# Performance work log

Measured on AMD Instinct MI355X. Metric: run time of the kernel, lower is better.

The kernel has to match this reference:

```python
import jax, jax.numpy as jnp
import numpy as np

EPS = 1e-5  # BatchNorm eps; eval-mode BN with running_mean=0, running_var=1 -> affine


def pe3d(C, x, y, z):
    """PositionalEncoding3D -> (C, x, y, z), faithfully reproducing the torch
    broadcasting (emb_x of shape (x,1,c) assigned into (x,y,z,c) slices)."""
    c = int(np.ceil(C / 3))
    inv_freq = jnp.asarray(1.0 / (10000.0 ** (np.arange(0, c, 2, dtype=np.float32) / c)))
    def emb(n):
        s = jnp.arange(n, dtype=jnp.float32)[:, None] * inv_freq[None, :]
        return jnp.concatenate([jnp.sin(s), jnp.cos(s)], axis=-1)  # (n, c)
    ex = emb(x)[:, None, :]   # (x,1,c) -> broadcasts as (1,x,1,c), same as torch
    ey = emb(y)[:, None, :]   # (y,1,c)
    ez = emb(z)               # (z,c)
    out = jnp.zeros((x, y, z, 3 * c), dtype=jnp.float32)
    out = out.at[..., :c].set(ex)
    out = out.at[..., c:2 * c].set(ey)
    out = out.at[..., 2 * c:3 * c].set(ez)
    return jnp.transpose(out[..., :C], (3, 0, 1, 2))  # (C,x,y,z)


def conv1x1(x, w, b):  # x:(B,Ci,D,H,W) w:(Co,Ci)
    return jnp.einsum('bcdhw,oc->bodhw', x, w) + b[None, :, None, None, None]


def bn_relu(x, g, b):  # eval BN (mean 0, var 1) + ReLU
    s = g / jnp.sqrt(1.0 + EPS)
    return jax.nn.relu(x * s[None, :, None, None, None] + b[None, :, None, None, None])


def setup_inputs() -> dict:
    key = jax.random.key(0)
    ks = jax.random.split(key, 16)
    B, Cy, Cs, D, H, W = 2, 96, 48, 16, 16, 16
    w = lambda k, shp: jax.random.normal(k, shp, dtype=jnp.float32) * 0.05
    return {
        'Y': jax.random.normal(ks[0], (B, Cy, D, H, W), dtype=jnp.float32),
        'S': jax.random.normal(ks[1], (B, Cs, D, H, W), dtype=jnp.float32),
        'w_s': w(ks[2], (Cs, Cs)), 'b_s': jnp.zeros((Cs,), jnp.float32),
        'g_s': jnp.ones((Cs,), jnp.float32), 'be_s': jnp.zeros((Cs,), jnp.float32),
        'w_y': w(ks[3], (Cs, Cy)), 'b_y': jnp.zeros((Cs,), jnp.float32),
        'g_y': jnp.ones((Cs,), jnp.float32), 'be_y': jnp.zeros((Cs,), jnp.float32),
        'Wq': w(ks[4], (Cs, Cs)), 'Wk': w(ks[5], (Cs, Cs)), 'Wv': w(ks[6], (Cs, Cs)),
        'w_o': w(ks[7], (Cs, Cs)), 'b_o': jnp.zeros((Cs,), jnp.float32),
        'g_o': jnp.ones((Cs,), jnp.float32), 'be_o': jnp.zeros((Cs,), jnp.float32),
        'w3': w(ks[8], (Cy, Cy, 3, 3, 3)), 'b3': jnp.zeros((Cy,), jnp.float32),
        'w_y2': w(ks[9], (Cs, Cy)), 'b_y2': jnp.zeros((Cs,), jnp.float32),
        'g_y2': jnp.ones((Cs,), jnp.float32), 'be_y2': jnp.zeros((Cs,), jnp.float32),
    }


def reference(Y, S, w_s, b_s, g_s, be_s, w_y, b_y, g_y, be_y, Wq, Wk, Wv,
              w_o, b_o, g_o, be_o, w3, b3, w_y2, b_y2, g_y2, be_y2):
    B, Cs, D, H, W = S.shape
    Cy = Y.shape[1]
    N = D * H * W
    # positional encodings (added, not learned)
    S = S + pe3d(Cs, D, H, W)[None]
    Y = Y + pe3d(Cy, D, H, W)[None]
    # projections: conv1x1 + BN + ReLU
    S1 = bn_relu(conv1x1(S, w_s, b_s), g_s, be_s).reshape(B, Cs, N).transpose(0, 2, 1)  # (B,N,Cs)
    Y1 = bn_relu(conv1x1(Y, w_y, b_y), g_y, be_y).reshape(B, Cs, N).transpose(0, 2, 1)  # (B,N,Cs)
    # Yconv2: 3x3x3 conv -> 1x1 conv -> BN -> ReLU
    Y3 = jax.lax.conv_general_dilated(Y, w3, (1, 1, 1), 'SAME',
                                      dimension_numbers=('NCDHW', 'OIDHW', 'NCDHW'))
    Y3 = Y3 + b3[None, :, None, None, None]
    Y2 = bn_relu(conv1x1(Y3, w_y2, b_y2), g_y2, be_y2)  # (B,Cs,D,H,W)
    # MultiHeadDense = plain right-matmul by (d,d) weight
    Q = jnp.einsum('bnd,de->bne', Y1, Wq)
    K = jnp.einsum('bnd,de->bne', Y1, Wk)
    V = jnp.einsum('bnd,de->bne', S1, Wv)
    # attention with NON-STANDARD softmax over axis=1 (queries, not keys)
    A = jax.nn.softmax(jnp.einsum('bqd,bkd->bqk', Q, K) * (float(Cs) ** -0.5), axis=1)
    x = jnp.einsum('bqk,bkd->bqd', A, V)                       # (B,N,Cs)
    x = x.transpose(0, 2, 1).reshape(B, Cs, D, H, W)
    Z = bn_relu(conv1x1(x, w_o, b_o), g_o, be_o) * S
    return jnp.concatenate([Z, Y2], axis=1)  # (B, 2*Cs, D, H, W)
```

## Files before the change

### kernel.cpp

```cpp
#include <hip/hip_runtime.h>
#include <hip/hip_bf16.h>

#define NPOS 4096
#define BB 2
#define KS2 32
#define QS2 32

typedef short v4s __attribute__((ext_vector_type(4)));
typedef short v8s __attribute__((ext_vector_type(8)));
typedef float v4f __attribute__((ext_vector_type(4)));
typedef unsigned short ushort_t;

static __device__ __forceinline__ unsigned short f2bf(float f) {
    unsigned int u = __float_as_uint(f);
    return (unsigned short)((u + 0x7fffu + ((u >> 16) & 1u)) >> 16);
}
static __device__ __forceinline__ float bf2f(ushort_t s) {
    return __uint_as_float(((unsigned int)s) << 16);
}

__device__ __forceinline__ float pe_val(int C, int c, int ch, int h, int w) {
    int blk = ch / c;
    int j = ch - blk * c;
    int half = c >> 1;
    int jj = (j < half) ? j : j - half;
    float freq = __expf(-(2.0f * jj / (float)c) * 9.210340371976184f);
    int pos = (blk < 2) ? h : w;
    float s = (float)pos * freq;
    return (j < half) ? __sinf(s) : __cosf(s);
}

__global__ void prep1_kernel(const float* __restrict__ S, const float* __restrict__ Y,
                             const float* __restrict__ w3, float* __restrict__ S_pe,
                             float* __restrict__ Y_pe, ushort_t* __restrict__ wr) {
    int bid = blockIdx.x;
    if (bid < 1536) {
        int idx = bid * 256 + threadIdx.x;
        int n = idx & 4095; int ch = (idx >> 12) % 48;
        S_pe[idx] = S[idx] + pe_val(48, 16, ch, (n >> 4) & 15, n & 15);
    } else if (bid < 4608) {
        int idx = (bid - 1536) * 256 + threadIdx.x;
        int n = idx & 4095; int ch = (idx >> 12) % 96;
        Y_pe[idx] = Y[idx] + pe_val(96, 32, ch, (n >> 4) & 15, n & 15);
    } else {
        int idx = (bid - 4608) * 256 + threadIdx.x;
        if (idx < 27 * 96 * 96) {
            int ci = idx % 96;
            int t2 = idx / 96;
            int co = t2 % 96;
            int tap = t2 / 96;
            wr[idx] = f2bf(w3[(size_t)(co * 96 + ci) * 27 + tap]);
        }
    }
}

template<int CI>
__device__ __forceinline__ void proj_body(int r, const float* __restrict__ in,
                                          const float* __restrict__ w, const float* __restrict__ bias,
                                          const float* __restrict__ g, const float* __restrict__ be,
                                          float* __restrict__ out) {
    int pc = r >> 3, cc = r & 7;
    int o0 = cc * 6;
    __shared__ float wl[6 * CI];
    __shared__ float sb[6], bb[6];
    int t = threadIdx.x;
    for (int i = t; i < 6 * CI; i += 256) {
        int o = i / CI, ci = i - o * CI;
        wl[i] = w[(size_t)(o0 + o) * CI + ci];
    }
    if (t < 6) {
        float s = g[o0 + t] * rsqrtf(1.0f + 1e-5f);
        sb[t] = s; bb[t] = bias[o0 + t] * s + be[o0 + t];
    }
    __syncthreads();
    int gn = pc * 256 + t;
    int b = gn >> 12;
    const float* ip = in + (size_t)b * CI * NPOS + (gn & 4095);
    float acc[6];
#pragma unroll
    for (int o = 0; o < 6; o++) acc[o] = 0.f;
#pragma unroll
    for (int ci = 0; ci < CI; ci++) {
        float v = ip[(size_t)ci * NPOS];
#pragma unroll
        for (int o = 0; o < 6; o++) acc[o] += v * wl[o * CI + ci];
    }
    float* op = out + (size_t)gn * 48 + o0;
#pragma unroll
    for (int o = 0; o < 6; o++) {
        float z = acc[o] * sb[o] + bb[o];
        op[o] = z > 0.f ? z : 0.f;
    }
}

__global__ void prep2_kernel(const float* __restrict__ Y_pe, const float* __restrict__ S_pe,
                             const float* __restrict__ w_s, const float* __restrict__ b_s,
                             const float* __restrict__ g_s, const float* __restrict__ be_s,
                             const float* __restrict__ w_y, const float* __restrict__ b_y,
                             const float* __restrict__ g_y, const float* __restrict__ be_y,
                             ushort_t* __restrict__ Ypad, float* __restrict__ S1,
                             float* __restrict__ Y1) {
    int bid = blockIdx.x;
    if (bid < 1094) {
        int idx = bid * 256 + threadIdx.x;
        if (idx >= BB * 5832 * 24) return;
        int ci4 = idx % 24;
        int cell = idx / 24;
        int wp = cell % 18; int c2 = cell / 18;
        int hp = c2 % 18; int c3 = c2 / 18;
        int zp = c3 % 18; int b = c3 / 18;
        ushort_t pk[4] = {0, 0, 0, 0};
        if (zp >= 1 && zp <= 16 && hp >= 1 && hp <= 16 && wp >= 1 && wp <= 16) {
            int n = (zp - 1) * 256 + (hp - 1) * 16 + (wp - 1);
#pragma unroll
            for (int j = 0; j < 4; j++)
                pk[j] = f2bf(Y_pe[((size_t)(b * 96 + ci4 * 4 + j) << 12) + n]);
        }
        *(v4s*)&Ypad[(size_t)idx * 4] = *(v4s*)pk;
    } else {
        int r = bid - 1094;
        if (r < 256) proj_body<48>(r, S_pe, w_s, b_s, g_s, be_s, S1);
        else proj_body<96>(r - 256, Y_pe, w_y, b_y, g_y, be_y, Y1);
    }
}

__global__ void qkv_kernel(const float* __restrict__ Y1, const float* __restrict__ S1,
                           const float* __restrict__ Wq, const float* __restrict__ Wk,
                           const float* __restrict__ Wv, ushort_t* __restrict__ Qb,
                           ushort_t* __restrict__ Kb, ushort_t* __restrict__ Vt) {
    int grp = blockIdx.x >> 8;
    int r = blockIdx.x & 255;
    int pc = r >> 3, cc = r & 7;
    int o0 = cc * 6;
    const float* in = (grp == 2) ? S1 : Y1;
    const float* w = (grp == 0) ? Wq : (grp == 1) ? Wk : Wv;
    __shared__ float wl[48 * 6];
    int t = threadIdx.x;
    for (int i = t; i < 48 * 6; i += 256) {
        int d = i / 6, o = i - d * 6;
        wl[i] = w[(size_t)d * 48 + o0 + o];
    }
    __syncthreads();
    int gn = pc * 256 + t;
    const float* ip = in + (size_t)gn * 48;
    float acc[6];
#pragma unroll
    for (int o = 0; o < 6; o++) acc[o] = 0.f;
#pragma unroll
    for (int d = 0; d < 48; d++) {
        float v = ip[d];
#pragma unroll
        for (int o = 0; o < 6; o++) acc[o] += v * wl[d * 6 + o];
    }
    if (grp < 2) {
        ushort_t* base = (grp == 0 ? Qb : Kb) + (size_t)gn * 64;
#pragma unroll
        for (int o = 0; o < 6; o++) base[o0 + o] = f2bf(acc[o]);
        if (cc == 0) {
            v8s z = {0, 0, 0, 0, 0, 0, 0, 0};
            *(v8s*)(base + 48) = z;
            *(v8s*)(base + 56) = z;
        }
    } else {
        int b = gn >> 12; int n = gn & 4095;
#pragma unroll
        for (int o = 0; o < 6; o++)
            Vt[((size_t)(b * 48 + o0 + o) << 12) + n] = f2bf(acc[o]);
    }
}

__global__ void attn_stats_mfma_kernel(const ushort_t* __restrict__ Qb,
                                       const ushort_t* __restrict__ Kb,
                                       float* __restrict__ ps) {
    int bid = blockIdx.x;
    int qs = bid & 31; int kb = (bid >> 5) & 15; int b = bid >> 9;
    int t = threadIdx.x; int wv = t >> 6; int lane = t & 63;
    int lr = lane & 15, g = lane >> 4;
    const float scale = 0.14433756729740643f;
    int key0 = kb * 256 + wv * 64;
    v8s ka[4][2];
#pragma unroll
    for (int kt = 0; kt < 4; kt++) {
        const ushort_t* krow = Kb + ((size_t)(b * NPOS + key0 + kt * 16 + lr)) * 64;
        ka[kt][0] = *(const v8s*)(krow + 8 * g);
        ka[kt][1] = *(const v8s*)(krow + 32 + 8 * g);
    }
    float s[4][4];
#pragma unroll
    for (int kt = 0; kt < 4; kt++)
#pragma unroll
        for (int r = 0; r < 4; r++) s[kt][r] = 0.f;
    for (int qt = 0; qt < 8; qt++) {
        int q = qs * 128 + qt * 16 + lr;
        const ushort_t* qrow = Qb + ((size_t)(b * NPOS + q)) * 64;
        v8s qf0 = *(const v8s*)(qrow + 8 * g);
        v8s qf1 = *(const v8s*)(qrow + 32 + 8 * g);
#pragma unroll
        for (int kt = 0; kt < 4; kt++) {
            v4f acc = {0.f, 0.f, 0.f, 0.f};
            acc = __builtin_amdgcn_mfma_f32_16x16x32_bf16(ka[kt][0], qf0, acc, 0, 0, 0);
            acc = __builtin_amdgcn_mfma_f32_16x16x32_bf16(ka[kt][1], qf1, acc, 0, 0, 0);
#pragma unroll
            for (int r = 0; r < 4; r++) s[kt][r] += __expf(acc[r] * scale);
        }
    }
#pragma unroll
    for (int off = 1; off < 16; off <<= 1)
#pragma unroll
        for (int kt = 0; kt < 4; kt++)
#pragma unroll
            for (int r = 0; r < 4; r++) s[kt][r] += __shfl_xor(s[kt][r], off);
    if (lr == 0) {
#pragma unroll
        for (int kt = 0; kt < 4; kt++) {
            int idx = (b * QS2 + qs) * NPOS + key0 + kt * 16 + 4 * g;
            v4f ss = {s[kt][0], s[kt][1], s[kt][2], s[kt][3]};
            *(v4f*)&ps[idx] = ss;
        }
    }
}

__global__ void norm_vscale_kernel(const float* __restrict__ ps, ushort_t* __restrict__ Vt) {
    int idx = blockIdx.x * 256 + threadIdx.x;
    if (idx >= BB * 4 * NPOS) return;
    int k = idx & 4095;
    int rest = idx >> 12;
    int dg = rest & 3; int b = rest >> 2;
    float s = 0.f;
#pragma unroll
    for (int qs = 0; qs < QS2; qs++) s += ps[(size_t)(b * QS2 + qs) * NPOS + k];
    float ci = 1.0f / s;
#pragma unroll
    for (int d = dg * 12; d < dg * 12 + 12; d++) {
        size_t a = ((size_t)(b * 48 + d) << 12) + k;
        Vt[a] = f2bf(bf2f(Vt[a]) * ci);
    }
}

__global__ void attn_pv_mfma_kernel(const ushort_t* __restrict__ Qb,
                                    const ushort_t* __restrict__ Kb,
                                    const ushort_t* __restrict__ Vt,
                                    ushort_t* __restrict__ xpart) {
    int bid = blockIdx.x;
    int ks = bid & 31; int qb = (bid >> 5) & 15; int b = bid >> 9;
    int t = threadIdx.x; int wv = t >> 6; int lane = t & 63;
    int lr = lane & 15, g = lane >> 4;
    const float scale = 0.14433756729740643f;
    int q0 = qb * 256 + wv * 64;
    v8s qf[4][2];
#pragma unroll
    for (int qt = 0; qt < 4; qt++) {
        const ushort_t* qrow = Qb + ((size_t)(b * NPOS + q0 + qt * 16 + lr)) * 64;
        qf[qt][0] = *(const v8s*)(qrow + 8 * g);
        qf[qt][1] = *(const v8s*)(qrow + 32 + 8 * g);
    }
    v4f xacc[4][3];
#pragma unroll
    for (int qt = 0; qt < 4; qt++)
#pragma unroll
        for (int nt = 0; nt < 3; nt++) xacc[qt][nt] = (v4f){0.f, 0.f, 0.f, 0.f};
    for (int kt = 0; kt < 2; kt++) {
        int kb0 = ks * 128 + kt * 64;
        v4s p[4][4];
#pragma unroll
        for (int tm = 0; tm < 4; tm++) {
            const ushort_t* krow = Kb + ((size_t)(b * NPOS + kb0 + 16 * tm + lr)) * 64;
            v8s ka0 = *(const v8s*)(krow + 8 * g);
            v8s ka1 = *(const v8s*)(krow + 32 + 8 * g);
#pragma unroll
            for (int qt = 0; qt < 4; qt++) {
                v4f acc = {0.f, 0.f, 0.f, 0.f};
                acc = __builtin_amdgcn_mfma_f32_16x16x32_bf16(ka0, qf[qt][0], acc, 0, 0, 0);
                acc = __builtin_amdgcn_mfma_f32_16x16x32_bf16(ka1, qf[qt][1], acc, 0, 0, 0);
                v4s pp;
#pragma unroll
                for (int r = 0; r < 4; r++)
                    pp[r] = (short)f2bf(__expf(acc[r] * scale));
                p[tm][qt] = pp;
            }
        }
#pragma unroll
        for (int nt = 0; nt < 3; nt++) {
            const ushort_t* vrow = Vt + ((size_t)(b * 48 + 16 * nt + lr) << 12) + kb0;
#pragma unroll
            for (int tm = 0; tm < 4; tm++) {
                v4s vf = *(const v4s*)(vrow + 16 * tm + 4 * g);
#pragma unroll
                for (int qt = 0; qt < 4; qt++)
                    xacc[qt][nt] = __builtin_amdgcn_mfma_f32_16x16x16bf16_1k(
                        p[tm][qt], vf, xacc[qt][nt], 0, 0, 0);
            }
        }
    }
#pragma unroll
    for (int qt = 0; qt < 4; qt++)
#pragma unroll
        for (int nt = 0; nt < 3; nt++)
#pragma unroll
            for (int r = 0; r < 4; r++)
                xpart[(((size_t)(b * KS2 + ks) << 12) + q0 + qt * 16 + 4 * g + r) * 48 + 16 * nt + lr] =
                    f2bf(xacc[qt][nt][r]);
}

__global__ void xreduce_kernel(const ushort_t* __restrict__ xpart, float* __restrict__ xsum) {
    int v = blockIdx.x * 256 + threadIdx.x;
    if (v >= BB * NPOS * 6) return;
    int b = v / (NPOS * 6);
    int rem8 = (v - b * NPOS * 6) * 8;
    float s[8];
#pragma unroll
    for (int j = 0; j < 8; j++) s[j] = 0.f;
    const ushort_t* base = xpart + (size_t)b * KS2 * NPOS * 48 + rem8;
#pragma unroll 4
    for (int ks = 0; ks < KS2; ks++) {
        v8s x = *(const v8s*)(base + (size_t)ks * NPOS * 48);
#pragma unroll
        for (int j = 0; j < 8; j++) s[j] += bf2f((ushort_t)x[j]);
    }
    float* op = xsum + (size_t)b * NPOS * 48 + rem8;
    v4f lo = {s[0], s[1], s[2], s[3]};
    v4f hi = {s[4], s[5], s[6], s[7]};
    *(v4f*)op = lo;
    *(v4f*)(op + 4) = hi;
}

__global__ __launch_bounds__(256, 2)
void conv3d_mfma_kernel(const ushort_t* __restrict__ Ypad,
                        const ushort_t* __restrict__ wr,
                        const float* __restrict__ b3,
                        float* __restrict__ Y3) {
    int bid = blockIdx.x;
    int b = bid / 384;
    int r = bid % 384;
    int cot = r % 6;
    int zhq = r / 6;
    int t = threadIdx.x; int wv = t >> 6; int lane = t & 63;
    int z = zhq >> 2;
    int h = (zhq & 3) * 4 + wv;
    int lr = lane & 15, g = lane >> 4;
    v4f acc[3];
#pragma unroll
    for (int kd = 0; kd < 3; kd++) acc[kd] = (v4f){0.f, 0.f, 0.f, 0.f};
    const ushort_t* wbase = wr + (size_t)(cot * 16 + lr) * 96 + 8 * g;
#pragma unroll
    for (int kd = 0; kd < 3; kd++) {
#pragma unroll
        for (int kh = 0; kh < 3; kh++) {
            const ushort_t* arow = Ypad + (((size_t)(b * 18 + z + kd) * 18 + h + kh) * 18 + lr) * 96 + 8 * g;
            int tap0 = (kd * 3 + kh) * 3;
            v8s af[3][3], bf[3][3];
#pragma unroll
            for (int kw = 0; kw < 3; kw++)
#pragma unroll
                for (int c = 0; c < 3; c++) {
                    af[kw][c] = *(const v8s*)(arow + kw * 96 + c * 32);
                    bf[kw][c] = *(const v8s*)(wbase + (size_t)(tap0 + kw) * 96 * 96 + c * 32);
                }
#pragma unroll
            for (int kw = 0; kw < 3; kw++)
#pragma unroll
                for (int c = 0; c < 3; c++)
                    acc[kd] = __builtin_amdgcn_mfma_f32_16x16x32_bf16(
                        af[kw][c], bf[kw][c], acc[kd], 0, 0, 0);
        }
    }
    float bv = b3[cot * 16 + lr];
    int pos = z * 256 + h * 16 + 4 * g;
#pragma unroll
    for (int r2 = 0; r2 < 4; r2++)
        Y3[(((size_t)b << 12) + pos + r2) * 96 + cot * 16 + lr] =
            acc[0][r2] + acc[1][r2] + acc[2][r2] + bv;
}

__device__ __forceinline__ void z_out_body(int r, const float* __restrict__ xsum,
                                           const float* __restrict__ w_o, const float* __restrict__ b_o,
                                           const float* __restrict__ g_o, const float* __restrict__ be_o,
                                           const float* __restrict__ S_pe, float* __restrict__ out) {
    int pc = r >> 3, cc = r & 7;
    int o0 = cc * 6;
    __shared__ float wl[6 * 48];
    __shared__ float sb[6], bb[6];
    int t = threadIdx.x;
    for (int i = t; i < 6 * 48; i += 256) {
        int o = i / 48, d = i - o * 48;
        wl[i] = w_o[(size_t)(o0 + o) * 48 + d];
    }
    if (t < 6) {
        float s = g_o[o0 + t] * rsqrtf(1.f + 1e-5f);
        sb[t] = s; bb[t] = b_o[o0 + t] * s + be_o[o0 + t];
    }
    __syncthreads();
    int gn = pc * 256 + t;
    int b = gn >> 12; int n = gn & 4095;
    const v4f* p = (const v4f*)(xsum + (size_t)gn * 48);
    float x[48];
#pragma unroll
    for (int d4 = 0; d4 < 12; d4++) {
        v4f v = p[d4];
#pragma unroll
        for (int j = 0; j < 4; j++) x[d4 * 4 + j] = v[j];
    }
#pragma unroll
    for (int o = 0; o < 6; o++) {
        float acc = 0.f;
#pragma unroll
        for (int d = 0; d < 48; d++) acc += wl[o * 48 + d] * x[d];
        float z = acc * sb[o] + bb[o];
        z = z > 0.f ? z : 0.f;
        out[((size_t)b * 96 + o0 + o) * NPOS + n] = z * S_pe[((size_t)b * 48 + o0 + o) * NPOS + n];
    }
}

__device__ __forceinline__ void y2_out_body(int r, const float* __restrict__ Y3,
                                            const float* __restrict__ w_y2, const float* __restrict__ b_y2,
                                            const float* __restrict__ g_y2, const float* __restrict__ be_y2,
                                            float* __restrict__ out) {
    int pc = r >> 3, cc = r & 7;
    int o0 = cc * 6;
    __shared__ float wl2[6 * 96];
    __shared__ float sb2[6], bb2[6];
    int t = threadIdx.x;
    for (int i = t; i < 6 * 96; i += 256) {
        int o = i / 96, ci = i - o * 96;
        wl2[i] = w_y2[(size_t)(o0 + o) * 96 + ci];
    }
    if (t < 6) {
        float s = g_y2[o0 + t] * rsqrtf(1.f + 1e-5f);
        sb2[t] = s; bb2[t] = b_y2[o0 + t] * s + be_y2[o0 + t];
    }
    __syncthreads();
    int gn = pc * 256 + t;
    int b = gn >> 12; int n = gn & 4095;
    const v4f* ip = (const v4f*)(Y3 + (size_t)gn * 96);
    float acc[6];
#pragma unroll
    for (int o = 0; o < 6; o++) acc[o] = 0.f;
#pragma unroll
    for (int c4 = 0; c4 < 24; c4++) {
        v4f v = ip[c4];
#pragma unroll
        for (int j = 0; j < 4; j++)
#pragma unroll
            for (int o = 0; o < 6; o++) acc[o] += v[j] * wl2[o * 96 + c4 * 4 + j];
    }
#pragma unroll
    for (int o = 0; o < 6; o++) {
        float z = acc[o] * sb2[o] + bb2[o];
        out[((size_t)b * 96 + 48 + o0 + o) * NPOS + n] = z > 0.f ? z : 0.f;
    }
}

__global__ void zy_out_kernel(const float* __restrict__ xsum, const float* __restrict__ w_o,
                              const float* __restrict__ b_o, const float* __restrict__ g_o,
                              const float* __restrict__ be_o, const float* __restrict__ S_pe,
                              const float* __restrict__ Y3, const float* __restrict__ w_y2,
                              const float* __restrict__ b_y2, const float* __restrict__ g_y2,
                              const float* __restrict__ be_y2, float* __restrict__ out) {
    int bid = blockIdx.x;
    if (bid < 256) z_out_body(bid, xsum, w_o, b_o, g_o, be_o, S_pe, out);
    else y2_out_body(bid - 256, Y3, w_y2, b_y2, g_y2, be_y2, out);
}

extern "C" void kernel_launch(void* const* d_in, const int* in_sizes, int n_in,
                              void* d_out, int out_size, void* d_ws, size_t ws_size,
                              hipStream_t stream) {
    const float* Y    = (const float*)d_in[0];
    const float* S    = (const float*)d_in[1];
    const float* w_s  = (const float*)d_in[2];
    const float* b_s  = (const float*)d_in[3];
    const float* g_s  = (const float*)d_in[4];
    const float* be_s = (const float*)d_in[5];
    const float* w_y  = (const float*)d_in[6];
    const float* b_y  = (const float*)d_in[7];
    const float* g_y  = (const float*)d_in[8];
    const float* be_y = (const float*)d_in[9];
    const float* Wq   = (const float*)d_in[10];
    const float* Wk   = (const float*)d_in[11];
    const float* Wv   = (const float*)d_in[12];
    const float* w_o  = (const float*)d_in[13];
    const float* b_o  = (const float*)d_in[14];
    const float* g_o  = (const float*)d_in[15];
    const float* be_o = (const float*)d_in[16];
    const float* w3   = (const float*)d_in[17];
    const float* b3   = (const float*)d_in[18];
    const float* w_y2 = (const float*)d_in[19];
    const float* b_y2 = (const float*)d_in[20];
    const float* g_y2 = (const float*)d_in[21];
    const float* be_y2= (const float*)d_in[22];
    float* out = (float*)d_out;

    float* ws = (float*)d_ws;
    float* S_pe   = ws;
    float* Y_pe   = ws + 393216;
    float* S1     = ws + 1179648;
    float* Y1     = ws + 1572864;
    ushort_t* Qb  = (ushort_t*)(ws + 1966080);
    ushort_t* Kb  = (ushort_t*)(ws + 2228224);
    ushort_t* Vt  = (ushort_t*)(ws + 2490368);
    float* ps     = ws + 2686976;
    ushort_t* xpart = (ushort_t*)(ws + 2949120);
    float* xsum   = ws + 9240576;
    float* Y3     = ws + 9633792;
    ushort_t* Ypad= (ushort_t*)(ws + 10420224);
    ushort_t* wr  = (ushort_t*)(ws + 10980096);

    prep1_kernel<<<5580, 256, 0, stream>>>(S, Y, w3, S_pe, Y_pe, wr);
    prep2_kernel<<<1606, 256, 0, stream>>>(Y_pe, S_pe, w_s, b_s, g_s, be_s,
                                           w_y, b_y, g_y, be_y, Ypad, S1, Y1);
    qkv_kernel<<<768, 256, 0, stream>>>(Y1, S1, Wq, Wk, Wv, Qb, Kb, Vt);
    attn_stats_mfma_kernel<<<BB * 16 * QS2, 256, 0, stream>>>(Qb, Kb, ps);
    norm_vscale_kernel<<<128, 256, 0, stream>>>(ps, Vt);
    attn_pv_mfma_kernel<<<BB * 16 * KS2, 256, 0, stream>>>(Qb, Kb, Vt, xpart);
    conv3d_mfma_kernel<<<768, 256, 0, stream>>>(Ypad, wr, b3, Y3);
    xreduce_kernel<<<192, 256, 0, stream>>>(xpart, xsum);
    zy_out_kernel<<<512, 256, 0, stream>>>(xsum, w_o, b_o, g_o, be_o, S_pe,
                                           Y3, w_y2, b_y2, g_y2, be_y2, out);
}
```

Measured before the change: 139.6 us.

## Merge attention PV and 3D conv into one launch; vectorize positional-encoding prep

The attention PV kernel and the 3x3x3 conv kernel become device functions dispatched by block index from a single launch. The two are independent, so their blocks can share the GPU and one launch boundary is removed. The prep kernel now handles four elements per thread with float4 loads and stores, and builds a small per-block table of positional-encoding values in shared memory instead of calling sin/cos for every element. In exchange, the merged kernel takes on the conv's launch bounds (256, 2) for the PV path too, which could change register allocation there.

```diff
diff --git a/kernel.cpp b/kernel.cpp
--- a/kernel.cpp
+++ b/kernel.cpp
@@ -34,16 +34,44 @@
                              const float* __restrict__ w3, float* __restrict__ S_pe,
                              float* __restrict__ Y_pe, ushort_t* __restrict__ wr) {
     int bid = blockIdx.x;
-    if (bid < 1536) {
-        int idx = bid * 256 + threadIdx.x;
-        int n = idx & 4095; int ch = (idx >> 12) % 48;
-        S_pe[idx] = S[idx] + pe_val(48, 16, ch, (n >> 4) & 15, n & 15);
-    } else if (bid < 4608) {
-        int idx = (bid - 1536) * 256 + threadIdx.x;
-        int n = idx & 4095; int ch = (idx >> 12) % 96;
-        Y_pe[idx] = Y[idx] + pe_val(96, 32, ch, (n >> 4) & 15, n & 15);
+    int t = threadIdx.x;
+    __shared__ float tb[16];
+    if (bid < 384) {
+        int idx4 = bid * 256 + t;
+        int ch = (idx4 >> 10) % 48;
+        if (t < 16) tb[t] = pe_val(48, 16, ch, t, t);
+        __syncthreads();
+        int n = (idx4 & 1023) * 4;
+        int h = (n >> 4) & 15, w0 = n & 15;
+        v4f x = *(const v4f*)&S[(size_t)idx4 * 4];
+        if (ch < 32) {
+            float p = tb[h];
+#pragma unroll
+            for (int j = 0; j < 4; j++) x[j] += p;
+        } else {
+#pragma unroll
+            for (int j = 0; j < 4; j++) x[j] += tb[w0 + j];
+        }
+        *(v4f*)&S_pe[(size_t)idx4 * 4] = x;
+    } else if (bid < 1152) {
+        int idx4 = (bid - 384) * 256 + t;
+        int ch = (idx4 >> 10) % 96;
+        if (t < 16) tb[t] = pe_val(96, 32, ch, t, t);
+        __syncthreads();
+        int n = (idx4 & 1023) * 4;
+        int h = (n >> 4) & 15, w0 = n & 15;
+        v4f x = *(const v4f*)&Y[(size_t)idx4 * 4];
+        if (ch < 64) {
+            float p = tb[h];
+#pragma unroll
+            for (int j = 0; j < 4; j++) x[j] += p;
+        } else {
+#pragma unroll
+            for (int j = 0; j < 4; j++) x[j] += tb[w0 + j];
+        }
+        *(v4f*)&Y_pe[(size_t)idx4 * 4] = x;
     } else {
-        int idx = (bid - 4608) * 256 + threadIdx.x;
+        int idx = (bid - 1152) * 256 + t;
         if (idx < 27 * 96 * 96) {
             int ci = idx % 96;
             int t2 = idx / 96;
@@ -237,11 +265,10 @@
     }
 }
 
-__global__ void attn_pv_mfma_kernel(const ushort_t* __restrict__ Qb,
-                                    const ushort_t* __restrict__ Kb,
-                                    const ushort_t* __restrict__ Vt,
-                                    ushort_t* __restrict__ xpart) {
-    int bid = blockIdx.x;
+__device__ __forceinline__ void pv_body(int bid, const ushort_t* __restrict__ Qb,
+                                        const ushort_t* __restrict__ Kb,
+                                        const ushort_t* __restrict__ Vt,
+                                        ushort_t* __restrict__ xpart) {
     int ks = bid & 31; int qb = (bid >> 5) & 15; int b = bid >> 9;
     int t = threadIdx.x; int wv = t >> 6; int lane = t & 63;
     int lr = lane & 15, g = lane >> 4;
@@ -302,34 +329,10 @@
                     f2bf(xacc[qt][nt][r]);
 }
 
-__global__ void xreduce_kernel(const ushort_t* __restrict__ xpart, float* __restrict__ xsum) {
-    int v = blockIdx.x * 256 + threadIdx.x;
-    if (v >= BB * NPOS * 6) return;
-    int b = v / (NPOS * 6);
-    int rem8 = (v - b * NPOS * 6) * 8;
-    float s[8];
-#pragma unroll
-    for (int j = 0; j < 8; j++) s[j] = 0.f;
-    const ushort_t* base = xpart + (size_t)b * KS2 * NPOS * 48 + rem8;
-#pragma unroll 4
-    for (int ks = 0; ks < KS2; ks++) {
-        v8s x = *(const v8s*)(base + (size_t)ks * NPOS * 48);
-#pragma unroll
-        for (int j = 0; j < 8; j++) s[j] += bf2f((ushort_t)x[j]);
-    }
-    float* op = xsum + (size_t)b * NPOS * 48 + rem8;
-    v4f lo = {s[0], s[1], s[2], s[3]};
-    v4f hi = {s[4], s[5], s[6], s[7]};
-    *(v4f*)op = lo;
-    *(v4f*)(op + 4) = hi;
-}
-
-__global__ __launch_bounds__(256, 2)
-void conv3d_mfma_kernel(const ushort_t* __restrict__ Ypad,
-                        const ushort_t* __restrict__ wr,
-                        const float* __restrict__ b3,
-                        float* __restrict__ Y3) {
-    int bid = blockIdx.x;
+__device__ __forceinline__ void conv_body(int bid, const ushort_t* __restrict__ Ypad,
+                                          const ushort_t* __restrict__ wr,
+                                          const float* __restrict__ b3,
+                                          float* __restrict__ Y3) {
     int b = bid / 384;
     int r = bid % 384;
     int cot = r % 6;
@@ -370,6 +373,38 @@
     for (int r2 = 0; r2 < 4; r2++)
         Y3[(((size_t)b << 12) + pos + r2) * 96 + cot * 16 + lr] =
             acc[0][r2] + acc[1][r2] + acc[2][r2] + bv;
+}
+
+__global__ __launch_bounds__(256, 2)
+void pvconv_kernel(const ushort_t* __restrict__ Qb, const ushort_t* __restrict__ Kb,
+                   const ushort_t* __restrict__ Vt, ushort_t* __restrict__ xpart,
+                   const ushort_t* __restrict__ Ypad, const ushort_t* __restrict__ wr,
+                   const float* __restrict__ b3, float* __restrict__ Y3) {
+    int bid = blockIdx.x;
+    if (bid < BB * 16 * KS2) pv_body(bid, Qb, Kb, Vt, xpart);
+    else conv_body(bid - BB * 16 * KS2, Ypad, wr, b3, Y3);
+}
+
+__global__ void xreduce_kernel(const ushort_t* __restrict__ xpart, float* __restrict__ xsum) {
+    int v = blockIdx.x * 256 + threadIdx.x;
+    if (v >= BB * NPOS * 6) return;
+    int b = v / (NPOS * 6);
+    int rem8 = (v - b * NPOS * 6) * 8;
+    float s[8];
+#pragma unroll
+    for (int j = 0; j < 8; j++) s[j] = 0.f;
+    const ushort_t* base = xpart + (size_t)b * KS2 * NPOS * 48 + rem8;
+#pragma unroll 4
+    for (int ks = 0; ks < KS2; ks++) {
+        v8s x = *(const v8s*)(base + (size_t)ks * NPOS * 48);
+#pragma unroll
+        for (int j = 0; j < 8; j++) s[j] += bf2f((ushort_t)x[j]);
+    }
+    float* op = xsum + (size_t)b * NPOS * 48 + rem8;
+    v4f lo = {s[0], s[1], s[2], s[3]};
+    v4f hi = {s[4], s[5], s[6], s[7]};
+    *(v4f*)op = lo;
+    *(v4f*)(op + 4) = hi;
 }
 
 __device__ __forceinline__ void z_out_body(int r, const float* __restrict__ xsum,
@@ -504,14 +539,14 @@
     ushort_t* Ypad= (ushort_t*)(ws + 10420224);
     ushort_t* wr  = (ushort_t*)(ws + 10980096);
 
-    prep1_kernel<<<5580, 256, 0, stream>>>(S, Y, w3, S_pe, Y_pe, wr);
+    prep1_kernel<<<2124, 256, 0, stream>>>(S, Y, w3, S_pe, Y_pe, wr);
     prep2_kernel<<<1606, 256, 0, stream>>>(Y_pe, S_pe, w_s, b_s, g_s, be_s,
                                            w_y, b_y, g_y, be_y, Ypad, S1, Y1);
     qkv_kernel<<<768, 256, 0, stream>>>(Y1, S1, Wq, Wk, Wv, Qb, Kb, Vt);
     attn_stats_mfma_kernel<<<BB * 16 * QS2, 256, 0, stream>>>(Qb, Kb, ps);
     norm_vscale_kernel<<<128, 256, 0, stream>>>(ps, Vt);
-    attn_pv_mfma_kernel<<<BB * 16 * KS2, 256, 0, stream>>>(Qb, Kb, Vt, xpart);
-    conv3d_mfma_kernel<<<768, 256, 0, stream>>>(Ypad, wr, b3, Y3);
+    pvconv_kernel<<<BB * 16 * KS2 + 768, 256, 0, stream>>>(Qb, Kb, Vt, xpart,
+                                                           Ypad, wr, b3, Y3);
     xreduce_kernel<<<192, 256, 0, stream>>>(xpart, xsum);
     zy_out_kernel<<<512, 256, 0, stream>>>(xsum, w_o, b_o, g_o, be_o, S_pe,
                                            Y3, w_y2, b_y2, g_y2, be_y2, out);
```

After: 136.9 us. No clear change (-2.0%).
